# Performance work log

Measured on AMD Instinct MI355X. Metric: run time of the kernel, lower is better.

The kernel has to match this reference:

```python
import jax, jax.numpy as jnp
import numpy as np
import math

N = 100000      # num_of_nodes
E = 1600000     # edges (~avg degree 16)
F = 128         # node_feature
D = 128         # node_hidden (also topK pool size)
NR = 90000      # remaining nodes
L = 2           # num_conv_layer
LAMDA = 0.5
ALPHA = 0.1


def setup_inputs() -> dict:
    key = jax.random.key(0)
    ks = jax.random.split(key, 12)
    g = lambda k, s: jax.random.normal(k, s, jnp.float32) * 0.05
    perm = np.random.RandomState(0).permutation(N)  # disjoint remain/added split
    return {
        "x": jax.random.normal(ks[0], (N, F), jnp.float32),
        "node_scores": jax.random.normal(ks[1], (N,), jnp.float32),
        "W_hid": g(ks[2], (F, D)), "b_hid": jnp.zeros((D,), jnp.float32),
        "Wl": g(ks[3], (D, D)), "bl": jnp.zeros((D,), jnp.float32),
        "Wr": g(ks[4], (D, D)), "br": jnp.zeros((D,), jnp.float32),
        "a": g(ks[5], (1, D)),
        "h0_w": g(ks[6], (D, D)),              # initial_weight (GRU hidden init / GCN weight)
        "W_ih": g(ks[7], (3 * D, D)), "W_hh": g(ks[8], (3 * D, D)),
        "b_ih": jnp.zeros((3 * D,), jnp.float32), "b_hh": jnp.zeros((3 * D,), jnp.float32),
        "edge_index": jax.random.randint(ks[9], (2, E), 0, N),
        "remain_nodes_index": jnp.asarray(perm[:NR], jnp.int32),
        "added_nodes_index": jnp.asarray(perm[NR:], jnp.int32),
        "node_id": jnp.arange(N, dtype=jnp.int32),
    }


def _gru_step(x_in, h, W_ih, W_hh, b_ih, b_hh):
    # torch nn.GRU single step, gate order (r, z, n)
    gx = x_in @ W_ih.T + b_ih
    gh = h @ W_hh.T + b_hh
    xr, xz, xn = jnp.split(gx, 3, axis=-1)
    hr, hz, hn = jnp.split(gh, 3, axis=-1)
    r = jax.nn.sigmoid(xr + hr)
    z = jax.nn.sigmoid(xz + hz)
    n = jnp.tanh(xn + r * hn)
    return (1.0 - z) * n + z * h


def _edge_softmax_weights(edge_index, a, h_l, h_r):
    # _dynamic_self_attention_v2: per-edge scores normalized over src rows
    src, dst = edge_index[0], edge_index[1]
    al = (jax.nn.leaky_relu(h_l, 0.2) * a).sum(-1)   # [N]
    ar = (jax.nn.leaky_relu(h_r, 0.2) * a).sum(-1)   # [N]
    e = al[src] + ar[dst]                            # [E]
    e = jnp.exp(e - e.max())
    rowsum = jax.ops.segment_sum(e, src, num_segments=h_l.shape[0])
    return e / (rowsum[src] + 1e-16)


def _spmm_adj_t(edge_index, w, feats):
    # (A_trans @ feats)[i] = sum over edges with dst==i of w_e * feats[src]
    src, dst = edge_index[0], edge_index[1]
    return jax.ops.segment_sum(w[:, None] * feats[src], dst, num_segments=feats.shape[0])


def reference(x, node_scores, W_hid, b_hid, Wl, bl, Wr, br, a, h0_w, W_ih, W_hh, b_ih, b_hh, edge_index, remain_nodes_index, added_nodes_index, node_id):
    h = jax.nn.relu(x @ W_hid + b_hid)                 # [N, D]
    remain_nodes = node_id[remain_nodes_index]
    remain_x = h[remain_nodes_index]
    added_nodes = node_id[added_nodes_index]
    added_x = h[added_nodes_index]
    scores = node_scores[remain_nodes_index]
    X_res = jnp.zeros((N, D), h.dtype)
    X_res = X_res.at[remain_nodes].set(remain_x).at[added_nodes].set(added_x)
    # topK pooling branch (N > D and NR > D statically)
    _, topk = jax.lax.top_k(scores, D)
    X_pool = remain_x[topk]                            # [D, D]: GRU batch=D, feat=D
    pooling_node = remain_nodes[topk]
    h_new = _gru_step(X_pool, h0_w, W_ih, W_hh, b_ih, b_hh)  # [D, D]
    # torch: X_GCN = X_residual (alias) then in-place scatter -> both updated
    X_res = X_res.at[pooling_node].set(h_new)
    X_gcn = X_res
    Wl_X = jax.nn.relu(X_gcn @ Wl + bl)
    Wr_X = jax.nn.relu(X_gcn @ Wr + br)
    w_edge = _edge_softmax_weights(edge_index, a, Wl_X, Wr_X)
    out = X_gcn
    for l in range(1, L + 1):
        theta = math.log(LAMDA / l + 1.0)
        hi = _spmm_adj_t(edge_index, w_edge, out)
        support = (1.0 - ALPHA) * hi + ALPHA * X_res
        out = jax.nn.relu(theta * (support @ h_new) + (1.0 - theta) * support)
    return out
```

## Files before the change

### kernel.cpp

```cpp
#include <hip/hip_runtime.h>

typedef unsigned int u32;
typedef unsigned short u16;
typedef unsigned long long u64;

#define DD 128
#define ELLW 64
#define NB 196
#define BSH 9
#define BCAP 12288

typedef __attribute__((ext_vector_type(8))) short short8;
typedef __attribute__((ext_vector_type(4))) float f32x4;
union fragu { uint4 q; short8 s; };

__device__ __forceinline__ u32 mono32(float f) {
    u32 u = __float_as_uint(f);
    return (u & 0x80000000u) ? ~u : (u | 0x80000000u);
}
__device__ __forceinline__ u16 f2bf(float f) {
    u32 u = __float_as_uint(f);
    u32 r = (u + 0x7FFFu + ((u >> 16) & 1u)) >> 16;
    return (u16)r;
}
__device__ __forceinline__ float bflo(u32 p) { return __uint_as_float(p << 16); }
__device__ __forceinline__ float bfhi(u32 p) { return __uint_as_float(p & 0xFFFF0000u); }

__device__ u32 block_incl_scan(u32 v, u32* wsum ) {
    int t = threadIdx.x, lane = t & 63, wid = t >> 6;
    u32 sc = v;
#pragma unroll
    for (int off = 1; off < 64; off <<= 1) {
        u32 n1 = __shfl_up(sc, off);
        if (lane >= off) sc += n1;
    }
    if (lane == 63) wsum[wid] = sc;
    __syncthreads();
    if (t < 16) {
        u32 wv = wsum[t];
#pragma unroll
        for (int off = 1; off < 16; off <<= 1) {
            u32 n1 = __shfl_up(wv, off, 16);
            if ((t & 15) >= off) wv += n1;
        }
        wsum[t] = wv;
    }
    __syncthreads();
    u32 r = sc + (wid ? wsum[wid - 1] : 0u);
    __syncthreads();
    return r;
}

template <int MODE, int ABF>
__global__ __launch_bounds__(256) void k_mfma(
    const void* __restrict__ Ain, const float* __restrict__ B,
    const float* __restrict__ bias, const float* __restrict__ av,
    const float* __restrict__ scaleS,
    u16* __restrict__ outBF, float* __restrict__ outF, float* __restrict__ outS,
    float theta, int N) {
    __shared__ alignas(16) unsigned char As[64 * 256];
    __shared__ float spart[64];
    int t = threadIdx.x, lane = t & 63, wave = t >> 6;
    int R0 = blockIdx.x * 64;
    int brow = (lane >> 4) * 8;
    int bcol0 = wave * 32 + (lane & 15);
    fragu bfr[2][4];
#pragma unroll
    for (int ntl = 0; ntl < 2; ++ntl)
#pragma unroll
        for (int ks = 0; ks < 4; ++ks) {
            u16 h[8];
#pragma unroll
            for (int i = 0; i < 8; ++i)
                h[i] = f2bf(B[(size_t)(ks * 32 + brow + i) * 128 + bcol0 + ntl * 16]);
            bfr[ntl][ks].q = make_uint4((u32)h[0] | ((u32)h[1] << 16), (u32)h[2] | ((u32)h[3] << 16),
                                        (u32)h[4] | ((u32)h[5] << 16), (u32)h[6] | ((u32)h[7] << 16));
        }
    float bc[2] = {0.f, 0.f}, ac[2] = {0.f, 0.f};
    if (MODE == 0 || MODE == 1) {
#pragma unroll
        for (int ntl = 0; ntl < 2; ++ntl) {
            bc[ntl] = bias[bcol0 + ntl * 16];
            if (MODE == 1) ac[ntl] = av[bcol0 + ntl * 16];
        }
    }
    if (MODE == 1 && t < 64) spart[t] = 0.f;
#pragma unroll
    for (int q2 = 0; q2 < 4; ++q2) {
        int c = t + q2 * 256;
        int row = c >> 4, c16 = c & 15;
        uint4 v = make_uint4(0u, 0u, 0u, 0u);
        if (R0 + row < N) {
            if (ABF) {
                v = ((const uint4*)Ain)[(size_t)(R0 + row) * 16 + c16];
            } else {
                float4 f0 = ((const float4*)Ain)[(size_t)(R0 + row) * 32 + c16 * 2];
                float4 f1 = ((const float4*)Ain)[(size_t)(R0 + row) * 32 + c16 * 2 + 1];
                v.x = (u32)f2bf(f0.x) | ((u32)f2bf(f0.y) << 16);
                v.y = (u32)f2bf(f0.z) | ((u32)f2bf(f0.w) << 16);
                v.z = (u32)f2bf(f1.x) | ((u32)f2bf(f1.y) << 16);
                v.w = (u32)f2bf(f1.z) | ((u32)f2bf(f1.w) << 16);
            }
        }
        *(uint4*)(As + row * 256 + ((c16 * 16) ^ ((row & 7) << 4))) = v;
    }
    __syncthreads();
    int arow = lane & 15, agrp = lane >> 4;
    float om = 1.f - theta;
#pragma unroll
    for (int rs = 0; rs < 4; ++rs) {
        int rl = rs * 16 + arow;
        fragu afr[4];
#pragma unroll
        for (int ks = 0; ks < 4; ++ks)
            afr[ks].q = *(const uint4*)(As + rl * 256 + ((ks * 64 + agrp * 16) ^ ((rl & 7) << 4)));
        float part[4] = {0.f, 0.f, 0.f, 0.f};
#pragma unroll
        for (int ntl = 0; ntl < 2; ++ntl) {
            f32x4 acc = {0.f, 0.f, 0.f, 0.f};
#pragma unroll
            for (int ks = 0; ks < 4; ++ks)
                acc = __builtin_amdgcn_mfma_f32_16x16x32_bf16(afr[ks].s, bfr[ntl][ks].s, acc, 0, 0, 0);
            int colg = wave * 32 + ntl * 16 + (lane & 15);
#pragma unroll
            for (int r = 0; r < 4; ++r) {
                int rowg = R0 + rs * 16 + agrp * 4 + r;
                if (MODE == 0) {
                    float v = fmaxf(acc[r] + bc[ntl], 0.f);
                    if (rowg < N) outBF[(size_t)rowg * 128 + colg] = f2bf(v);
                } else if (MODE == 1) {
                    part[r] += fmaxf(acc[r] + bc[ntl], 0.f) * ac[ntl];
                } else {
                    int rl2 = rs * 16 + agrp * 4 + r;
                    u16 rh = *(const u16*)(As + rl2 * 256 + ((colg * 2) ^ ((rl2 & 7) << 4)));
                    float resid = __uint_as_float((u32)rh << 16);
                    float v = fmaxf(theta * acc[r] + om * resid, 0.f);
                    if (rowg < N) {
                        if (MODE == 2) {
                            float rsc = 1.f / (scaleS[rowg] + 1e-30f);
                            outBF[(size_t)rowg * 128 + colg] = f2bf(v * rsc);
                        } else {
                            outF[(size_t)rowg * 128 + colg] = v;
                        }
                    }
                }
            }
        }
        if (MODE == 1) {
#pragma unroll
            for (int r = 0; r < 4; ++r) {
                float s = part[r];
                s += __shfl_xor(s, 1); s += __shfl_xor(s, 2);
                s += __shfl_xor(s, 4); s += __shfl_xor(s, 8);
                if ((lane & 15) == 0) atomicAdd(&spart[rs * 16 + agrp * 4 + r], s);
            }
        }
    }
    if (MODE == 1) {
        __syncthreads();
        if (t < 64 && R0 + t < N) outS[R0 + t] = expf(spart[t]);
    }
}

__global__ void k_init(u32* __restrict__ curD, u32* __restrict__ curS) {
    int t = blockIdx.x * blockDim.x + threadIdx.x;
    if (t < NB) { curD[t] = (u32)t * BCAP; curS[t] = (u32)t * BCAP; }
}

__global__ __launch_bounds__(256) void k_bucket(
    const int* __restrict__ ei, u64* __restrict__ bD, u64* __restrict__ bS,
    u32* __restrict__ curD, u32* __restrict__ curS, int E, int nblocks) {
    __shared__ u32 cnt0[NB], cnt1[NB], pos0[NB], pos1[NB], base0[NB], base1[NB];
    int t = threadIdx.x;
    int chunk = (E + nblocks - 1) / nblocks;
    int e0 = blockIdx.x * chunk, e1 = min(E, e0 + chunk);
    for (int i = t; i < NB; i += 256) { cnt0[i] = 0; cnt1[i] = 0; pos0[i] = 0; pos1[i] = 0; }
    __syncthreads();
    for (int e = e0 + t; e < e1; e += 256) {
        int s = ei[e], d = ei[E + e];
        atomicAdd(&cnt0[d >> BSH], 1u);
        atomicAdd(&cnt1[s >> BSH], 1u);
    }
    __syncthreads();
    for (int i = t; i < NB; i += 256) {
        base0[i] = atomicAdd(&curD[i], cnt0[i]);
        base1[i] = atomicAdd(&curS[i], cnt1[i]);
    }
    __syncthreads();
    for (int e = e0 + t; e < e1; e += 256) {
        int s = ei[e], d = ei[E + e];
        int bd = d >> BSH, bs = s >> BSH;
        u32 pD = base0[bd] + atomicAdd(&pos0[bd], 1u);
        u32 pS = base1[bs] + atomicAdd(&pos1[bs], 1u);
        if (pD < (u32)(bd + 1) * BCAP) bD[pD] = ((u64)(u32)d << 32) | (u32)s;
        if (pS < (u32)(bs + 1) * BCAP) bS[pS] = ((u64)(u32)s << 32) | (u32)d;
    }
}

__global__ __launch_bounds__(256) void k_ell(
    const u64* __restrict__ bD, const u32* __restrict__ curD,
    int* __restrict__ ell, u32* __restrict__ cnt, int N) {
    __shared__ u32 lcnt[512];
    int b = blockIdx.x, t = threadIdx.x;
    for (int i = t; i < 512; i += 256) lcnt[i] = 0;
    __syncthreads();
    u32 beg = (u32)b * BCAP, end = curD[b];
    for (u32 e = beg + t; e < end; e += 256) {
        u64 p = bD[e];
        int d = (int)(p >> 32), s = (int)(u32)p;
        u32 q = atomicAdd(&lcnt[d & 511], 1u);
        if (q < (u32)ELLW) ell[((size_t)d << 6) + q] = s;
    }
    __syncthreads();
    int r0 = b << BSH;
    for (int i = t; i < 512; i += 256) {
        int row = r0 + i;
        if (row < N) cnt[row] = min(lcnt[i], (u32)ELLW);
    }
}

__global__ __launch_bounds__(256) void k_S(
    const u64* __restrict__ bS, const u32* __restrict__ curS,
    const float* __restrict__ ear, float* __restrict__ S, int N) {
    __shared__ float ls[512];
    int b = blockIdx.x, t = threadIdx.x;
    for (int i = t; i < 512; i += 256) ls[i] = 0.f;
    __syncthreads();
    u32 beg = (u32)b * BCAP, end = curS[b];
    for (u32 e = beg + t; e < end; e += 256) {
        u64 p = bS[e];
        int s = (int)(p >> 32), d = (int)(u32)p;
        atomicAdd(&ls[s & 511], ear[d]);
    }
    __syncthreads();
    int r0 = b << BSH;
    for (int i = t; i < 512; i += 256) {
        int row = r0 + i;
        if (row < N) S[row] = ls[i];
    }
}

__global__ void k_scale(const u32* __restrict__ Xrbf, const float* __restrict__ S,
                        u32* __restrict__ out_bf, int N) {
    int idx = blockIdx.x * blockDim.x + threadIdx.x;
    if (idx >= N * 64) return;
    int row = idx >> 6;
    float rs = 1.f / (S[row] + 1e-30f);
    u32 p = Xrbf[idx];
    out_bf[idx] = (u32)f2bf(bflo(p) * rs) | ((u32)f2bf(bfhi(p) * rs) << 16);
}

__global__ __launch_bounds__(256) void k_spmm(
    const u32* __restrict__ featsc, const u32* __restrict__ xr_bf,
    const float* __restrict__ ear, const u32* __restrict__ cnt,
    const int* __restrict__ ell, u32* __restrict__ sup_bf, int N) {
    int w = (int)((blockIdx.x * (u32)blockDim.x + threadIdx.x) >> 6);
    int lane = threadIdx.x & 63;
    if (w >= N) return;
    int m = (int)min(cnt[w], (u32)ELLW);
    int sv = (lane < m) ? ell[((size_t)w << 6) + lane] : 0;
    float a0 = 0.f, a1 = 0.f;
    int j = 0;
    for (; j + 8 <= m; j += 8) {
        int s0 = __shfl(sv, j + 0), s1 = __shfl(sv, j + 1);
        int s2 = __shfl(sv, j + 2), s3 = __shfl(sv, j + 3);
        int s4 = __shfl(sv, j + 4), s5 = __shfl(sv, j + 5);
        int s6 = __shfl(sv, j + 6), s7 = __shfl(sv, j + 7);
        u32 p0 = featsc[(size_t)s0 * 64 + lane];
        u32 p1 = featsc[(size_t)s1 * 64 + lane];
        u32 p2 = featsc[(size_t)s2 * 64 + lane];
        u32 p3 = featsc[(size_t)s3 * 64 + lane];
        u32 p4 = featsc[(size_t)s4 * 64 + lane];
        u32 p5 = featsc[(size_t)s5 * 64 + lane];
        u32 p6 = featsc[(size_t)s6 * 64 + lane];
        u32 p7 = featsc[(size_t)s7 * 64 + lane];
        a0 += bflo(p0) + bflo(p1) + bflo(p2) + bflo(p3) + bflo(p4) + bflo(p5) + bflo(p6) + bflo(p7);
        a1 += bfhi(p0) + bfhi(p1) + bfhi(p2) + bfhi(p3) + bfhi(p4) + bfhi(p5) + bfhi(p6) + bfhi(p7);
    }
    for (; j + 2 <= m; j += 2) {
        int s0 = __shfl(sv, j + 0), s1 = __shfl(sv, j + 1);
        u32 p0 = featsc[(size_t)s0 * 64 + lane];
        u32 p1 = featsc[(size_t)s1 * 64 + lane];
        a0 += bflo(p0) + bflo(p1);
        a1 += bfhi(p0) + bfhi(p1);
    }
    if (j < m) {
        int s0 = __shfl(sv, j);
        u32 p0 = featsc[(size_t)s0 * 64 + lane];
        a0 += bflo(p0);
        a1 += bfhi(p0);
    }
    float sc = 0.9f * ear[w];
    u32 xp = xr_bf[(size_t)w * 64 + lane];
    float o0 = sc * a0 + 0.1f * bflo(xp);
    float o1 = sc * a1 + 0.1f * bfhi(xp);
    sup_bf[(size_t)w * 64 + lane] = (u32)f2bf(o0) | ((u32)f2bf(o1) << 16);
}

__global__ void k_hist(const float* __restrict__ scores, const int* __restrict__ remain,
                       u32* __restrict__ hist, int NR) {
    int i = blockIdx.x * blockDim.x + threadIdx.x;
    if (i < NR) atomicAdd(&hist[mono32(scores[remain[i]]) >> 16], 1u);
}

__global__ void k_cutoff(const u32* __restrict__ hist, u32* __restrict__ misc, int K) {
    __shared__ u32 wsum[16];
    __shared__ u32 carry_s, found_s;
    int t = threadIdx.x;
    if (t == 0) { carry_s = 0; found_s = 0; }
    __syncthreads();
    for (int c = 0; c < 64; ++c) {
        int key = 65535 - ((c << 10) + t);
        u32 v = hist[key];
        u32 carry = carry_s;
        __syncthreads();
        u32 incl = block_incl_scan(v, wsum);
        u32 mycum = carry + incl;
        u32 myprev = mycum - v;
        if (mycum >= (u32)K && myprev < (u32)K) {
            misc[2] = (u32)key;
            misc[3] = myprev;
            found_s = 1;
        }
        if (t == 1023) carry_s = mycum;
        __syncthreads();
        if (found_s) return;
    }
}

__global__ void k_collect(const float* __restrict__ scores, const int* __restrict__ remain,
                          const u32* __restrict__ misc, int* __restrict__ cand,
                          u32* __restrict__ cand_cnt, int NR, int CMAX) {
    u32 B = misc[2];
    int i = blockIdx.x * blockDim.x + threadIdx.x;
    if (i < NR) {
        u32 b = mono32(scores[remain[i]]) >> 16;
        if (b >= B) {
            u32 p = atomicAdd(cand_cnt, 1u);
            if (p < (u32)CMAX) cand[p] = i;
        }
    }
}

__global__ void k_select(const float* __restrict__ scores, const int* __restrict__ remain,
                         const u32* __restrict__ misc, const int* __restrict__ cand,
                         int* __restrict__ pooling, int K, int CMAX) {
    __shared__ u64 keys[4096];
    int n = (int)min(misc[0], (u32)CMAX);
    int t = threadIdx.x;
    for (int c = t; c < n; c += 1024) {
        int i = cand[c];
        u32 m = mono32(scores[remain[i]]);
        keys[c] = ((u64)m << 32) | (u64)(0xFFFFFFFFu - (u32)i);
    }
    __syncthreads();
    for (int c = t; c < n; c += 1024) {
        u64 myk = keys[c];
        int rank = 0;
        for (int j = 0; j < n; ++j) rank += (keys[j] > myk) ? 1 : 0;
        if (rank < K) pooling[rank] = remain[cand[c]];
    }
}

__global__ void k_gru(const u16* __restrict__ Xh, const int* __restrict__ pooling,
                      const float* __restrict__ h0w, const float* __restrict__ Wih,
                      const float* __restrict__ Whh, const float* __restrict__ bih,
                      const float* __restrict__ bhh, float* __restrict__ hnew) {
    __shared__ float xrow[DD], hrow[DD];
    int j = blockIdx.x, t = threadIdx.x;
    int node = pooling[j];
    xrow[t] = __uint_as_float((u32)Xh[(size_t)node * DD + t] << 16);
    hrow[t] = h0w[j * DD + t];
    __syncthreads();
    float gx[3], gh[3];
#pragma unroll
    for (int g = 0; g < 3; ++g) {
        const float* wi = Wih + (g * DD + t) * DD;
        const float* wh = Whh + (g * DD + t) * DD;
        float ax = bih[g * DD + t];
        float ah = bhh[g * DD + t];
        for (int d = 0; d < DD; ++d) {
            ax += xrow[d] * wi[d];
            ah += hrow[d] * wh[d];
        }
        gx[g] = ax; gh[g] = ah;
    }
    float r = 1.f / (1.f + expf(-(gx[0] + gh[0])));
    float z = 1.f / (1.f + expf(-(gx[1] + gh[1])));
    float nn = tanhf(gx[2] + r * gh[2]);
    hnew[j * DD + t] = (1.f - z) * nn + z * hrow[t];
}

__global__ void k_scatter(u32* __restrict__ Xr_bf, const int* __restrict__ pooling,
                          const float* __restrict__ hnew) {
    int j = blockIdx.x, t = threadIdx.x;
    int row = pooling[j];
    float2 f = ((const float2*)hnew)[j * 64 + t];
    Xr_bf[(size_t)row * 64 + t] = (u32)f2bf(f.x) | ((u32)f2bf(f.y) << 16);
}

extern "C" void kernel_launch(void* const* d_in, const int* in_sizes, int n_in,
                              void* d_out, int out_size, void* d_ws, size_t ws_size,
                              hipStream_t stream) {
    const float* x    = (const float*)d_in[0];
    const float* nsc  = (const float*)d_in[1];
    const float* Wh   = (const float*)d_in[2];
    const float* bh   = (const float*)d_in[3];
    const float* Wr   = (const float*)d_in[6];
    const float* br   = (const float*)d_in[7];
    const float* av   = (const float*)d_in[8];
    const float* h0w  = (const float*)d_in[9];
    const float* Wih  = (const float*)d_in[10];
    const float* Whh  = (const float*)d_in[11];
    const float* bih  = (const float*)d_in[12];
    const float* bhh  = (const float*)d_in[13];
    const int* ei     = (const int*)d_in[14];
    const int* remain = (const int*)d_in[15];

    int N = in_sizes[1];
    int E = in_sizes[14] / 2;
    int NR = in_sizes[15];
    const int K = DD;
    const int CMAX = 4096;
    int mblocks = (N + 63) / 64;
    const int NBLK = 512;

    char* ws = (char*)d_ws;
    size_t off = 0;
    auto alloc = [&](size_t bytes) -> size_t {
        off = (off + 255) & ~(size_t)255;
        size_t o = off;
        off += bytes;
        return o;
    };
    size_t bucket_bytes = (size_t)2 * NB * BCAP * 8;
    size_t sup_bytes = (size_t)N * 64 * 4;
    size_t o_Xrbf = alloc((size_t)N * 64 * 4);
    size_t o_Xsc  = alloc((size_t)N * 64 * 4);
    size_t o_Abf  = alloc((size_t)N * 64 * 4);
    size_t o_sup  = alloc(bucket_bytes > sup_bytes ? bucket_bytes : sup_bytes);
    size_t o_ear  = alloc((size_t)N * 4);
    size_t o_ell  = alloc((size_t)N * ELLW * 4);
    size_t o_cand = alloc((size_t)CMAX * 4);
    size_t o_pool = alloc((size_t)K * 4);
    size_t o_hnew = alloc((size_t)DD * DD * 4);
    size_t o_S    = alloc((size_t)N * 4);
    size_t o_cnt  = alloc((size_t)N * 4);
    size_t o_cur  = alloc((size_t)2 * 256 * 4);
    size_t o_hist = alloc((size_t)65536 * 4);
    size_t o_misc = alloc((size_t)64 * 4);
    size_t zero_len = (o_misc + 64 * 4) - o_hist;
    (void)ws_size; (void)n_in; (void)out_size;

    u32*   Xrbf = (u32*)(ws + o_Xrbf);
    u32*   Xsc  = (u32*)(ws + o_Xsc);
    u32*   Abf  = (u32*)(ws + o_Abf);
    u32*   supb = (u32*)(ws + o_sup);
    u64*   bD   = (u64*)(ws + o_sup);
    u64*   bS   = (u64*)(ws + o_sup + (size_t)NB * BCAP * 8);
    float* ear  = (float*)(ws + o_ear);
    int*   ell  = (int*)(ws + o_ell);
    int*   cand = (int*)(ws + o_cand);
    int*   pool = (int*)(ws + o_pool);
    float* hnew = (float*)(ws + o_hnew);
    float* S    = (float*)(ws + o_S);
    u32*   cnt  = (u32*)(ws + o_cnt);
    u32*   curD = (u32*)(ws + o_cur);
    u32*   curS = (u32*)(ws + o_cur + 256 * 4);
    u32*   hist = (u32*)(ws + o_hist);
    u32*   misc = (u32*)(ws + o_misc);

    const float theta1 = 0.40546510810816438f;
    const float theta2 = 0.22314355131420976f;

    hipMemsetAsync(ws + o_hist, 0, zero_len, stream);

    k_mfma<0, 0><<<mblocks, 256, 0, stream>>>(x, Wh, bh, nullptr, nullptr,
                                              (u16*)Xrbf, nullptr, nullptr, 0.f, N);
    k_hist<<<(NR + 255) / 256, 256, 0, stream>>>(nsc, remain, hist, NR);
    k_cutoff<<<1, 1024, 0, stream>>>(hist, misc, K);
    k_collect<<<(NR + 255) / 256, 256, 0, stream>>>(nsc, remain, misc, cand, misc, NR, CMAX);
    k_select<<<1, 1024, 0, stream>>>(nsc, remain, misc, cand, pool, K, CMAX);
    k_gru<<<K, DD, 0, stream>>>((const u16*)Xrbf, pool, h0w, Wih, Whh, bih, bhh, hnew);
    k_scatter<<<K, 64, 0, stream>>>(Xrbf, pool, hnew);
    k_mfma<1, 1><<<mblocks, 256, 0, stream>>>(Xrbf, Wr, br, av, nullptr,
                                              nullptr, nullptr, ear, 0.f, N);
    k_init<<<1, 256, 0, stream>>>(curD, curS);
    k_bucket<<<NBLK, 256, 0, stream>>>(ei, bD, bS, curD, curS, E, NBLK);
    k_ell<<<NB, 256, 0, stream>>>(bD, curD, ell, cnt, N);
    k_S<<<NB, 256, 0, stream>>>(bS, curS, ear, S, N);
    k_scale<<<(N * 64 + 255) / 256, 256, 0, stream>>>(Xrbf, S, Xsc, N);
    k_spmm<<<(N + 3) / 4, 256, 0, stream>>>(Xsc, Xrbf, ear, cnt, ell, supb, N);
    k_mfma<2, 1><<<mblocks, 256, 0, stream>>>(supb, hnew, nullptr, nullptr, S,
                                              (u16*)Abf, nullptr, nullptr, theta1, N);
    k_spmm<<<(N + 3) / 4, 256, 0, stream>>>(Abf, Xrbf, ear, cnt, ell, supb, N);
    k_mfma<3, 1><<<mblocks, 256, 0, stream>>>(supb, hnew, nullptr, nullptr, nullptr,
                                              nullptr, (float*)d_out, nullptr, theta2, N);
}
```

Before: 382.5 us.

## Fuse SpMM gather into MFMA layer kernel and fold row scaling into S kernel

Result: slower. 522.7 us (+36.6%).

```diff
diff --git a/kernel.cpp b/kernel.cpp
--- a/kernel.cpp
+++ b/kernel.cpp
@@ -55,9 +55,7 @@
 __global__ __launch_bounds__(256) void k_mfma(
     const void* __restrict__ Ain, const float* __restrict__ B,
     const float* __restrict__ bias, const float* __restrict__ av,
-    const float* __restrict__ scaleS,
-    u16* __restrict__ outBF, float* __restrict__ outF, float* __restrict__ outS,
-    float theta, int N) {
+    u16* __restrict__ outBF, float* __restrict__ outS, int N) {
     __shared__ alignas(16) unsigned char As[64 * 256];
     __shared__ float spart[64];
     int t = threadIdx.x, lane = t & 63, wave = t >> 6;
@@ -76,13 +74,11 @@
             bfr[ntl][ks].q = make_uint4((u32)h[0] | ((u32)h[1] << 16), (u32)h[2] | ((u32)h[3] << 16),
                                         (u32)h[4] | ((u32)h[5] << 16), (u32)h[6] | ((u32)h[7] << 16));
         }
-    float bc[2] = {0.f, 0.f}, ac[2] = {0.f, 0.f};
-    if (MODE == 0 || MODE == 1) {
-#pragma unroll
-        for (int ntl = 0; ntl < 2; ++ntl) {
-            bc[ntl] = bias[bcol0 + ntl * 16];
-            if (MODE == 1) ac[ntl] = av[bcol0 + ntl * 16];
-        }
+    float bc[2], ac[2] = {0.f, 0.f};
+#pragma unroll
+    for (int ntl = 0; ntl < 2; ++ntl) {
+        bc[ntl] = bias[bcol0 + ntl * 16];
+        if (MODE == 1) ac[ntl] = av[bcol0 + ntl * 16];
     }
     if (MODE == 1 && t < 64) spart[t] = 0.f;
 #pragma unroll
@@ -106,7 +102,6 @@
     }
     __syncthreads();
     int arow = lane & 15, agrp = lane >> 4;
-    float om = 1.f - theta;
 #pragma unroll
     for (int rs = 0; rs < 4; ++rs) {
         int rl = rs * 16 + arow;
@@ -128,21 +123,8 @@
                 if (MODE == 0) {
                     float v = fmaxf(acc[r] + bc[ntl], 0.f);
                     if (rowg < N) outBF[(size_t)rowg * 128 + colg] = f2bf(v);
-                } else if (MODE == 1) {
+                } else {
                     part[r] += fmaxf(acc[r] + bc[ntl], 0.f) * ac[ntl];
-                } else {
-                    int rl2 = rs * 16 + agrp * 4 + r;
-                    u16 rh = *(const u16*)(As + rl2 * 256 + ((colg * 2) ^ ((rl2 & 7) << 4)));
-                    float resid = __uint_as_float((u32)rh << 16);
-                    float v = fmaxf(theta * acc[r] + om * resid, 0.f);
-                    if (rowg < N) {
-                        if (MODE == 2) {
-                            float rsc = 1.f / (scaleS[rowg] + 1e-30f);
-                            outBF[(size_t)rowg * 128 + colg] = f2bf(v * rsc);
-                        } else {
-                            outF[(size_t)rowg * 128 + colg] = v;
-                        }
-                    }
                 }
             }
         }
@@ -159,6 +141,97 @@
     if (MODE == 1) {
         __syncthreads();
         if (t < 64 && R0 + t < N) outS[R0 + t] = expf(spart[t]);
+    }
+}
+
+template <int MODE>
+__global__ __launch_bounds__(256) void k_layer(
+    const u32* __restrict__ feat, const u32* __restrict__ xrbf,
+    const float* __restrict__ ear, const u32* __restrict__ cnt,
+    const int* __restrict__ ell, const float* __restrict__ B,
+    const float* __restrict__ scaleS,
+    u16* __restrict__ outBF, float* __restrict__ outF, float theta, int N) {
+    __shared__ alignas(16) unsigned char As[64 * 256];
+    int t = threadIdx.x, lane = t & 63, wave = t >> 6;
+    int R0 = blockIdx.x * 64;
+    for (int r = 0; r < 16; ++r) {
+        int rowl = wave * 16 + r;
+        int rowg = R0 + rowl;
+        float a0 = 0.f, a1 = 0.f;
+        u32 pk = 0u;
+        if (rowg < N) {
+            int m = (int)min(cnt[rowg], (u32)ELLW);
+            const int* rowp = ell + ((size_t)rowg << 6);
+            int j = 0;
+            for (; j + 8 <= m; j += 8) {
+                u32 pv[8];
+#pragma unroll
+                for (int q = 0; q < 8; ++q) {
+                    int s = rowp[j + q];
+                    pv[q] = feat[(size_t)s * 64 + lane];
+                }
+#pragma unroll
+                for (int q = 0; q < 8; ++q) { a0 += bflo(pv[q]); a1 += bfhi(pv[q]); }
+            }
+            for (; j < m; ++j) {
+                int s = rowp[j];
+                u32 p = feat[(size_t)s * 64 + lane];
+                a0 += bflo(p); a1 += bfhi(p);
+            }
+            float sc = 0.9f * ear[rowg];
+            u32 xp = xrbf[(size_t)rowg * 64 + lane];
+            float o0 = sc * a0 + 0.1f * bflo(xp);
+            float o1 = sc * a1 + 0.1f * bfhi(xp);
+            pk = (u32)f2bf(o0) | ((u32)f2bf(o1) << 16);
+        }
+        *(u32*)(As + rowl * 256 + ((lane * 4) ^ ((rowl & 7) << 4))) = pk;
+    }
+    int brow = (lane >> 4) * 8, bcol0 = wave * 32 + (lane & 15);
+    fragu bfr[2][4];
+#pragma unroll
+    for (int ntl = 0; ntl < 2; ++ntl)
+#pragma unroll
+        for (int ks = 0; ks < 4; ++ks) {
+            u16 h[8];
+#pragma unroll
+            for (int i = 0; i < 8; ++i)
+                h[i] = f2bf(B[(size_t)(ks * 32 + brow + i) * 128 + bcol0 + ntl * 16]);
+            bfr[ntl][ks].q = make_uint4((u32)h[0] | ((u32)h[1] << 16), (u32)h[2] | ((u32)h[3] << 16),
+                                        (u32)h[4] | ((u32)h[5] << 16), (u32)h[6] | ((u32)h[7] << 16));
+        }
+    __syncthreads();
+    int arow = lane & 15, agrp = lane >> 4;
+    float om = 1.f - theta;
+#pragma unroll
+    for (int rs = 0; rs < 4; ++rs) {
+        int rl = rs * 16 + arow;
+        fragu afr[4];
+#pragma unroll
+        for (int ks = 0; ks < 4; ++ks)
+            afr[ks].q = *(const uint4*)(As + rl * 256 + ((ks * 64 + agrp * 16) ^ ((rl & 7) << 4)));
+#pragma unroll
+        for (int ntl = 0; ntl < 2; ++ntl) {
+            f32x4 acc = {0.f, 0.f, 0.f, 0.f};
+#pragma unroll
+            for (int ks = 0; ks < 4; ++ks)
+                acc = __builtin_amdgcn_mfma_f32_16x16x32_bf16(afr[ks].s, bfr[ntl][ks].s, acc, 0, 0, 0);
+            int colg = wave * 32 + ntl * 16 + (lane & 15);
+#pragma unroll
+            for (int r = 0; r < 4; ++r) {
+                int rowg = R0 + rs * 16 + agrp * 4 + r;
+                if (rowg >= N) continue;
+                int rl2 = rs * 16 + agrp * 4 + r;
+                u16 rh = *(const u16*)(As + rl2 * 256 + ((colg * 2) ^ ((rl2 & 7) << 4)));
+                float resid = __uint_as_float((u32)rh << 16);
+                float v = fmaxf(theta * acc[r] + om * resid, 0.f);
+                if (MODE == 2) {
+                    float rsc = 1.f / (scaleS[rowg] + 1e-30f);
+                    outBF[(size_t)rowg * 128 + colg] = f2bf(v * rsc);
+                } else {
+                    outF[(size_t)rowg * 128 + colg] = v;
+                }
+            }
+        }
     }
 }
 
@@ -219,9 +292,10 @@
     }
 }
 
-__global__ __launch_bounds__(256) void k_S(
+__global__ __launch_bounds__(256) void k_Ssc(
     const u64* __restrict__ bS, const u32* __restrict__ curS,
-    const float* __restrict__ ear, float* __restrict__ S, int N) {
+    const float* __restrict__ ear, const u32* __restrict__ Xrbf,
+    float* __restrict__ S, u32* __restrict__ Xsc, int N) {
     __shared__ float ls[512];
     int b = blockIdx.x, t = threadIdx.x;
     for (int i = t; i < 512; i += 256) ls[i] = 0.f;
@@ -238,63 +312,15 @@
         int row = r0 + i;
         if (row < N) S[row] = ls[i];
     }
-}
-
-__global__ void k_scale(const u32* __restrict__ Xrbf, const float* __restrict__ S,
-                        u32* __restrict__ out_bf, int N) {
-    int idx = blockIdx.x * blockDim.x + threadIdx.x;
-    if (idx >= N * 64) return;
-    int row = idx >> 6;
-    float rs = 1.f / (S[row] + 1e-30f);
-    u32 p = Xrbf[idx];
-    out_bf[idx] = (u32)f2bf(bflo(p) * rs) | ((u32)f2bf(bfhi(p) * rs) << 16);
-}
-
-__global__ __launch_bounds__(256) void k_spmm(
-    const u32* __restrict__ featsc, const u32* __restrict__ xr_bf,
-    const float* __restrict__ ear, const u32* __restrict__ cnt,
-    const int* __restrict__ ell, u32* __restrict__ sup_bf, int N) {
-    int w = (int)((blockIdx.x * (u32)blockDim.x + threadIdx.x) >> 6);
-    int lane = threadIdx.x & 63;
-    if (w >= N) return;
-    int m = (int)min(cnt[w], (u32)ELLW);
-    int sv = (lane < m) ? ell[((size_t)w << 6) + lane] : 0;
-    float a0 = 0.f, a1 = 0.f;
-    int j = 0;
-    for (; j + 8 <= m; j += 8) {
-        int s0 = __shfl(sv, j + 0), s1 = __shfl(sv, j + 1);
-        int s2 = __shfl(sv, j + 2), s3 = __shfl(sv, j + 3);
-        int s4 = __shfl(sv, j + 4), s5 = __shfl(sv, j + 5);
-        int s6 = __shfl(sv, j + 6), s7 = __shfl(sv, j + 7);
-        u32 p0 = featsc[(size_t)s0 * 64 + lane];
-        u32 p1 = featsc[(size_t)s1 * 64 + lane];
-        u32 p2 = featsc[(size_t)s2 * 64 + lane];
-        u32 p3 = featsc[(size_t)s3 * 64 + lane];
-        u32 p4 = featsc[(size_t)s4 * 64 + lane];
-        u32 p5 = featsc[(size_t)s5 * 64 + lane];
-        u32 p6 = featsc[(size_t)s6 * 64 + lane];
-        u32 p7 = featsc[(size_t)s7 * 64 + lane];
-        a0 += bflo(p0) + bflo(p1) + bflo(p2) + bflo(p3) + bflo(p4) + bflo(p5) + bflo(p6) + bflo(p7);
-        a1 += bfhi(p0) + bfhi(p1) + bfhi(p2) + bfhi(p3) + bfhi(p4) + bfhi(p5) + bfhi(p6) + bfhi(p7);
-    }
-    for (; j + 2 <= m; j += 2) {
-        int s0 = __shfl(sv, j + 0), s1 = __shfl(sv, j + 1);
-        u32 p0 = featsc[(size_t)s0 * 64 + lane];
-        u32 p1 = featsc[(size_t)s1 * 64 + lane];
-        a0 += bflo(p0) + bflo(p1);
-        a1 += bfhi(p0) + bfhi(p1);
-    }
-    if (j < m) {
-        int s0 = __shfl(sv, j);
-        u32 p0 = featsc[(size_t)s0 * 64 + lane];
-        a0 += bflo(p0);
-        a1 += bfhi(p0);
-    }
-    float sc = 0.9f * ear[w];
-    u32 xp = xr_bf[(size_t)w * 64 + lane];
-    float o0 = sc * a0 + 0.1f * bflo(xp);
-    float o1 = sc * a1 + 0.1f * bfhi(xp);
-    sup_bf[(size_t)w * 64 + lane] = (u32)f2bf(o0) | ((u32)f2bf(o1) << 16);
+    int rows = min(512, N - r0);
+    if (rows <= 0) return;
+    for (int idx = t; idx < rows * 64; idx += 256) {
+        int row = r0 + (idx >> 6);
+        float rs = 1.f / (ls[idx >> 6] + 1e-30f);
+        u32 p = Xrbf[(size_t)row * 64 + (idx & 63)];
+        Xsc[(size_t)row * 64 + (idx & 63)] =
+            (u32)f2bf(bflo(p) * rs) | ((u32)f2bf(bfhi(p) * rs) << 16);
+    }
 }
 
 __global__ void k_hist(const float* __restrict__ scores, const int* __restrict__ remain,
@@ -433,12 +459,10 @@
         off += bytes;
         return o;
     };
-    size_t bucket_bytes = (size_t)2 * NB * BCAP * 8;
-    size_t sup_bytes = (size_t)N * 64 * 4;
     size_t o_Xrbf = alloc((size_t)N * 64 * 4);
     size_t o_Xsc  = alloc((size_t)N * 64 * 4);
     size_t o_Abf  = alloc((size_t)N * 64 * 4);
-    size_t o_sup  = alloc(bucket_bytes > sup_bytes ? bucket_bytes : sup_bytes);
+    size_t o_bkt  = alloc((size_t)2 * NB * BCAP * 8);
     size_t o_ear  = alloc((size_t)N * 4);
     size_t o_ell  = alloc((size_t)N * ELLW * 4);
     size_t o_cand = alloc((size_t)CMAX * 4);
@@ -455,9 +479,8 @@
     u32*   Xrbf = (u32*)(ws + o_Xrbf);
     u32*   Xsc  = (u32*)(ws + o_Xsc);
     u32*   Abf  = (u32*)(ws + o_Abf);
-    u32*   supb = (u32*)(ws + o_sup);
-    u64*   bD   = (u64*)(ws + o_sup);
-    u64*   bS   = (u64*)(ws + o_sup + (size_t)NB * BCAP * 8);
+    u64*   bD   = (u64*)(ws + o_bkt);
+    u64*   bS   = (u64*)(ws + o_bkt + (size_t)NB * BCAP * 8);
     float* ear  = (float*)(ws + o_ear);
     int*   ell  = (int*)(ws + o_ell);
     int*   cand = (int*)(ws + o_cand);
@@ -475,25 +498,20 @@
 
     hipMemsetAsync(ws + o_hist, 0, zero_len, stream);
 
-    k_mfma<0, 0><<<mblocks, 256, 0, stream>>>(x, Wh, bh, nullptr, nullptr,
-                                              (u16*)Xrbf, nullptr, nullptr, 0.f, N);
+    k_mfma<0, 0><<<mblocks, 256, 0, stream>>>(x, Wh, bh, nullptr, (u16*)Xrbf, nullptr, N);
     k_hist<<<(NR + 255) / 256, 256, 0, stream>>>(nsc, remain, hist, NR);
     k_cutoff<<<1, 1024, 0, stream>>>(hist, misc, K);
     k_collect<<<(NR + 255) / 256, 256, 0, stream>>>(nsc, remain, misc, cand, misc, NR, CMAX);
     k_select<<<1, 1024, 0, stream>>>(nsc, remain, misc, cand, pool, K, CMAX);
     k_gru<<<K, DD, 0, stream>>>((const u16*)Xrbf, pool, h0w, Wih, Whh, bih, bhh, hnew);
     k_scatter<<<K, 64, 0, stream>>>(Xrbf, pool, hnew);
-    k_mfma<1, 1><<<mblocks, 256, 0, stream>>>(Xrbf, Wr, br, av, nullptr,
-                                              nullptr, nullptr, ear, 0.f, N);
+    k_mfma<1, 1><<<mblocks, 256, 0, stream>>>(Xrbf, Wr, br, av, nullptr, ear, N);
     k_init<<<1, 256, 0, stream>>>(curD, curS);
     k_bucket<<<NBLK, 256, 0, stream>>>(ei, bD, bS, curD, curS, E, NBLK);
     k_ell<<<NB, 256, 0, stream>>>(bD, curD, ell, cnt, N);
-    k_S<<<NB, 256, 0, stream>>>(bS, curS, ear, S, N);
-    k_scale<<<(N * 64 + 255) / 256, 256, 0, stream>>>(Xrbf, S, Xsc, N);
-    k_spmm<<<(N + 3) / 4, 256, 0, stream>>>(Xsc, Xrbf, ear, cnt, ell, supb, N);
-    k_mfma<2, 1><<<mblocks, 256, 0, stream>>>(supb, hnew, nullptr, nullptr, S,
-                                              (u16*)Abf, nullptr, nullptr, theta1, N);
-    k_spmm<<<(N + 3) / 4, 256, 0, stream>>>(Abf, Xrbf, ear, cnt, ell, supb, N);
-    k_mfma<3, 1><<<mblocks, 256, 0, stream>>>(supb, hnew, nullptr, nullptr, nullptr,
-                                              nullptr, (float*)d_out, nullptr, theta2, N);
-}
+    k_Ssc<<<NB, 256, 0, stream>>>(bS, curS, ear, Xrbf, S, Xsc, N);
+    k_layer<2><<<mblocks, 256, 0, stream>>>(Xsc, Xrbf, ear, cnt, ell, hnew, S,
+                                            (u16*)Abf, nullptr, theta1, N);
+    k_layer<3><<<mblocks, 256, 0, stream>>>(Abf, Xrbf, ear, cnt, ell, hnew, nullptr,
+                                            nullptr, (float*)d_out, theta2, N);
+}
```

## Slice SpMM features into column-sliced layout and fuse scaling and residual

Applied to the files above, without the earlier changes.

After: 463.4 us. 1.21x slower.

```diff
diff --git a/kernel.cpp b/kernel.cpp
--- a/kernel.cpp
+++ b/kernel.cpp
@@ -25,6 +25,9 @@
 }
 __device__ __forceinline__ float bflo(u32 p) { return __uint_as_float(p << 16); }
 __device__ __forceinline__ float bfhi(u32 p) { return __uint_as_float(p & 0xFFFF0000u); }
+__device__ __forceinline__ u32 packbf(float a, float b) {
+    return (u32)f2bf(a) | ((u32)f2bf(b) << 16);
+}
 
 __device__ u32 block_incl_scan(u32 v, u32* wsum ) {
     int t = threadIdx.x, lane = t & 63, wid = t >> 6;
@@ -53,9 +56,9 @@
 
 template <int MODE, int ABF>
 __global__ __launch_bounds__(256) void k_mfma(
-    const void* __restrict__ Ain, const float* __restrict__ B,
-    const float* __restrict__ bias, const float* __restrict__ av,
-    const float* __restrict__ scaleS,
+    const void* __restrict__ Ain, const u32* __restrict__ resid,
+    const float* __restrict__ B, const float* __restrict__ bias,
+    const float* __restrict__ av, const float* __restrict__ scaleS,
     u16* __restrict__ outBF, float* __restrict__ outF, float* __restrict__ outS,
     float theta, int N) {
     __shared__ alignas(16) unsigned char As[64 * 256];
@@ -91,15 +94,22 @@
         int row = c >> 4, c16 = c & 15;
         uint4 v = make_uint4(0u, 0u, 0u, 0u);
         if (R0 + row < N) {
-            if (ABF) {
+            if (ABF == 1) {
                 v = ((const uint4*)Ain)[(size_t)(R0 + row) * 16 + c16];
+            } else if (ABF == 2) {
+                uint4 pv = ((const uint4*)Ain)[(size_t)(R0 + row) * 16 + c16];
+                uint4 xv = ((const uint4*)resid)[(size_t)(R0 + row) * 16 + c16];
+                v.x = packbf(bflo(pv.x) + 0.1f * bflo(xv.x), bfhi(pv.x) + 0.1f * bfhi(xv.x));
+                v.y = packbf(bflo(pv.y) + 0.1f * bflo(xv.y), bfhi(pv.y) + 0.1f * bfhi(xv.y));
+                v.z = packbf(bflo(pv.z) + 0.1f * bflo(xv.z), bfhi(pv.z) + 0.1f * bfhi(xv.z));
+                v.w = packbf(bflo(pv.w) + 0.1f * bflo(xv.w), bfhi(pv.w) + 0.1f * bfhi(xv.w));
             } else {
                 float4 f0 = ((const float4*)Ain)[(size_t)(R0 + row) * 32 + c16 * 2];
                 float4 f1 = ((const float4*)Ain)[(size_t)(R0 + row) * 32 + c16 * 2 + 1];
-                v.x = (u32)f2bf(f0.x) | ((u32)f2bf(f0.y) << 16);
-                v.y = (u32)f2bf(f0.z) | ((u32)f2bf(f0.w) << 16);
-                v.z = (u32)f2bf(f1.x) | ((u32)f2bf(f1.y) << 16);
-                v.w = (u32)f2bf(f1.z) | ((u32)f2bf(f1.w) << 16);
+                v.x = packbf(f0.x, f0.y);
+                v.y = packbf(f0.z, f0.w);
+                v.z = packbf(f1.x, f1.y);
+                v.w = packbf(f1.z, f1.w);
             }
         }
         *(uint4*)(As + row * 256 + ((c16 * 16) ^ ((row & 7) << 4))) = v;
@@ -133,12 +143,12 @@
                 } else {
                     int rl2 = rs * 16 + agrp * 4 + r;
                     u16 rh = *(const u16*)(As + rl2 * 256 + ((colg * 2) ^ ((rl2 & 7) << 4)));
-                    float resid = __uint_as_float((u32)rh << 16);
-                    float v = fmaxf(theta * acc[r] + om * resid, 0.f);
+                    float resv = __uint_as_float((u32)rh << 16);
+                    float v = fmaxf(theta * acc[r] + om * resv, 0.f);
                     if (rowg < N) {
                         if (MODE == 2) {
                             float rsc = 1.f / (scaleS[rowg] + 1e-30f);
-                            outBF[(size_t)rowg * 128 + colg] = f2bf(v * rsc);
+                            outBF[((size_t)(colg >> 4) * N + rowg) * 16 + (colg & 15)] = f2bf(v * rsc);
                         } else {
                             outF[(size_t)rowg * 128 + colg] = v;
                         }
@@ -160,6 +170,45 @@
         __syncthreads();
         if (t < 64 && R0 + t < N) outS[R0 + t] = expf(spart[t]);
     }
+}
+
+__global__ __launch_bounds__(256) void k_spmm(
+    const u32* __restrict__ featS, const float* __restrict__ ear,
+    const u32* __restrict__ cnt, const int* __restrict__ ell,
+    u32* __restrict__ P, int N) {
+    int slice = blockIdx.x & 7;
+    int chunk = blockIdx.x >> 3;
+    int lane = threadIdx.x & 63, wave = threadIdx.x >> 6;
+    int r8 = lane >> 3, c8 = lane & 7;
+    int row = chunk * 32 + wave * 8 + r8;
+    if (row >= N) return;
+    int m = (int)min(cnt[row], (u32)ELLW);
+    const int* rowp = ell + ((size_t)row << 6);
+    const u32* fbase = featS + (size_t)slice * N * 8 + c8;
+    float a0 = 0.f, a1 = 0.f;
+    int j = 0;
+    for (; j + 8 <= m; j += 8) {
+        int idx = rowp[j + c8];
+        u32 pv[8];
+#pragma unroll
+        for (int q = 0; q < 8; ++q) {
+            int s = __shfl(idx, q, 8);
+            pv[q] = fbase[(size_t)s * 8];
+        }
+#pragma unroll
+        for (int q = 0; q < 8; ++q) { a0 += bflo(pv[q]); a1 += bfhi(pv[q]); }
+    }
+    int rem = m - j;
+    if (rem > 0) {
+        int idx = (c8 < rem) ? rowp[j + c8] : 0;
+        for (int q = 0; q < rem; ++q) {
+            int s = __shfl(idx, q, 8);
+            u32 p = fbase[(size_t)s * 8];
+            a0 += bflo(p); a1 += bfhi(p);
+        }
+    }
+    float sc = 0.9f * ear[row];
+    P[(size_t)row * 64 + slice * 8 + c8] = packbf(sc * a0, sc * a1);
 }
 
 __global__ void k_init(u32* __restrict__ curD, u32* __restrict__ curS) {
@@ -219,9 +268,10 @@
     }
 }
 
-__global__ __launch_bounds__(256) void k_S(
+__global__ __launch_bounds__(256) void k_Ssc(
     const u64* __restrict__ bS, const u32* __restrict__ curS,
-    const float* __restrict__ ear, float* __restrict__ S, int N) {
+    const float* __restrict__ ear, const u32* __restrict__ Xrbf,
+    float* __restrict__ S, u32* __restrict__ XscS, int N) {
     __shared__ float ls[512];
     int b = blockIdx.x, t = threadIdx.x;
     for (int i = t; i < 512; i += 256) ls[i] = 0.f;
@@ -238,63 +288,16 @@
         int row = r0 + i;
         if (row < N) S[row] = ls[i];
     }
-}
-
-__global__ void k_scale(const u32* __restrict__ Xrbf, const float* __restrict__ S,
-                        u32* __restrict__ out_bf, int N) {
-    int idx = blockIdx.x * blockDim.x + threadIdx.x;
-    if (idx >= N * 64) return;
-    int row = idx >> 6;
-    float rs = 1.f / (S[row] + 1e-30f);
-    u32 p = Xrbf[idx];
-    out_bf[idx] = (u32)f2bf(bflo(p) * rs) | ((u32)f2bf(bfhi(p) * rs) << 16);
-}
-
-__global__ __launch_bounds__(256) void k_spmm(
-    const u32* __restrict__ featsc, const u32* __restrict__ xr_bf,
-    const float* __restrict__ ear, const u32* __restrict__ cnt,
-    const int* __restrict__ ell, u32* __restrict__ sup_bf, int N) {
-    int w = (int)((blockIdx.x * (u32)blockDim.x + threadIdx.x) >> 6);
-    int lane = threadIdx.x & 63;
-    if (w >= N) return;
-    int m = (int)min(cnt[w], (u32)ELLW);
-    int sv = (lane < m) ? ell[((size_t)w << 6) + lane] : 0;
-    float a0 = 0.f, a1 = 0.f;
-    int j = 0;
-    for (; j + 8 <= m; j += 8) {
-        int s0 = __shfl(sv, j + 0), s1 = __shfl(sv, j + 1);
-        int s2 = __shfl(sv, j + 2), s3 = __shfl(sv, j + 3);
-        int s4 = __shfl(sv, j + 4), s5 = __shfl(sv, j + 5);
-        int s6 = __shfl(sv, j + 6), s7 = __shfl(sv, j + 7);
-        u32 p0 = featsc[(size_t)s0 * 64 + lane];
-        u32 p1 = featsc[(size_t)s1 * 64 + lane];
-        u32 p2 = featsc[(size_t)s2 * 64 + lane];
-        u32 p3 = featsc[(size_t)s3 * 64 + lane];
-        u32 p4 = featsc[(size_t)s4 * 64 + lane];
-        u32 p5 = featsc[(size_t)s5 * 64 + lane];
-        u32 p6 = featsc[(size_t)s6 * 64 + lane];
-        u32 p7 = featsc[(size_t)s7 * 64 + lane];
-        a0 += bflo(p0) + bflo(p1) + bflo(p2) + bflo(p3) + bflo(p4) + bflo(p5) + bflo(p6) + bflo(p7);
-        a1 += bfhi(p0) + bfhi(p1) + bfhi(p2) + bfhi(p3) + bfhi(p4) + bfhi(p5) + bfhi(p6) + bfhi(p7);
-    }
-    for (; j + 2 <= m; j += 2) {
-        int s0 = __shfl(sv, j + 0), s1 = __shfl(sv, j + 1);
-        u32 p0 = featsc[(size_t)s0 * 64 + lane];
-        u32 p1 = featsc[(size_t)s1 * 64 + lane];
-        a0 += bflo(p0) + bflo(p1);
-        a1 += bfhi(p0) + bfhi(p1);
-    }
-    if (j < m) {
-        int s0 = __shfl(sv, j);
-        u32 p0 = featsc[(size_t)s0 * 64 + lane];
-        a0 += bflo(p0);
-        a1 += bfhi(p0);
-    }
-    float sc = 0.9f * ear[w];
-    u32 xp = xr_bf[(size_t)w * 64 + lane];
-    float o0 = sc * a0 + 0.1f * bflo(xp);
-    float o1 = sc * a1 + 0.1f * bfhi(xp);
-    sup_bf[(size_t)w * 64 + lane] = (u32)f2bf(o0) | ((u32)f2bf(o1) << 16);
+    int rows = min(512, N - r0);
+    if (rows <= 0) return;
+    for (int idx = t; idx < rows * 64; idx += 256) {
+        int rl = idx >> 6, c = idx & 63;
+        int row = r0 + rl;
+        float rs = 1.f / (ls[rl] + 1e-30f);
+        u32 p = Xrbf[(size_t)row * 64 + c];
+        XscS[((size_t)(c >> 3) * N + row) * 8 + (c & 7)] =
+            packbf(bflo(p) * rs, bfhi(p) * rs);
+    }
 }
 
 __global__ void k_hist(const float* __restrict__ scores, const int* __restrict__ remain,
@@ -396,7 +399,7 @@
     int j = blockIdx.x, t = threadIdx.x;
     int row = pooling[j];
     float2 f = ((const float2*)hnew)[j * 64 + t];
-    Xr_bf[(size_t)row * 64 + t] = (u32)f2bf(f.x) | ((u32)f2bf(f.y) << 16);
+    Xr_bf[(size_t)row * 64 + t] = packbf(f.x, f.y);
 }
 
 extern "C" void kernel_launch(void* const* d_in, const int* in_sizes, int n_in,
@@ -423,6 +426,7 @@
     const int K = DD;
     const int CMAX = 4096;
     int mblocks = (N + 63) / 64;
+    int sblocks = 8 * ((N + 31) / 32);
     const int NBLK = 512;
 
     char* ws = (char*)d_ws;
@@ -455,7 +459,7 @@
     u32*   Xrbf = (u32*)(ws + o_Xrbf);
     u32*   Xsc  = (u32*)(ws + o_Xsc);
     u32*   Abf  = (u32*)(ws + o_Abf);
-    u32*   supb = (u32*)(ws + o_sup);
+    u32*   P    = (u32*)(ws + o_sup);
     u64*   bD   = (u64*)(ws + o_sup);
     u64*   bS   = (u64*)(ws + o_sup + (size_t)NB * BCAP * 8);
     float* ear  = (float*)(ws + o_ear);
@@ -475,7 +479,7 @@
 
     hipMemsetAsync(ws + o_hist, 0, zero_len, stream);
 
-    k_mfma<0, 0><<<mblocks, 256, 0, stream>>>(x, Wh, bh, nullptr, nullptr,
+    k_mfma<0, 0><<<mblocks, 256, 0, stream>>>(x, nullptr, Wh, bh, nullptr, nullptr,
                                               (u16*)Xrbf, nullptr, nullptr, 0.f, N);
     k_hist<<<(NR + 255) / 256, 256, 0, stream>>>(nsc, remain, hist, NR);
     k_cutoff<<<1, 1024, 0, stream>>>(hist, misc, K);
@@ -483,17 +487,16 @@
     k_select<<<1, 1024, 0, stream>>>(nsc, remain, misc, cand, pool, K, CMAX);
     k_gru<<<K, DD, 0, stream>>>((const u16*)Xrbf, pool, h0w, Wih, Whh, bih, bhh, hnew);
     k_scatter<<<K, 64, 0, stream>>>(Xrbf, pool, hnew);
-    k_mfma<1, 1><<<mblocks, 256, 0, stream>>>(Xrbf, Wr, br, av, nullptr,
+    k_mfma<1, 1><<<mblocks, 256, 0, stream>>>(Xrbf, nullptr, Wr, br, av, nullptr,
                                               nullptr, nullptr, ear, 0.f, N);
     k_init<<<1, 256, 0, stream>>>(curD, curS);
     k_bucket<<<NBLK, 256, 0, stream>>>(ei, bD, bS, curD, curS, E, NBLK);
     k_ell<<<NB, 256, 0, stream>>>(bD, curD, ell, cnt, N);
-    k_S<<<NB, 256, 0, stream>>>(bS, curS, ear, S, N);
-    k_scale<<<(N * 64 + 255) / 256, 256, 0, stream>>>(Xrbf, S, Xsc, N);
-    k_spmm<<<(N + 3) / 4, 256, 0, stream>>>(Xsc, Xrbf, ear, cnt, ell, supb, N);
-    k_mfma<2, 1><<<mblocks, 256, 0, stream>>>(supb, hnew, nullptr, nullptr, S,
+    k_Ssc<<<NB, 256, 0, stream>>>(bS, curS, ear, Xrbf, S, Xsc, N);
+    k_spmm<<<sblocks, 256, 0, stream>>>(Xsc, ear, cnt, ell, P, N);
+    k_mfma<2, 2><<<mblocks, 256, 0, stream>>>(P, Xrbf, hnew, nullptr, nullptr, S,
                                               (u16*)Abf, nullptr, nullptr, theta1, N);
-    k_spmm<<<(N + 3) / 4, 256, 0, stream>>>(Abf, Xrbf, ear, cnt, ell, supb, N);
-    k_mfma<3, 1><<<mblocks, 256, 0, stream>>>(supb, hnew, nullptr, nullptr, nullptr,
+    k_spmm<<<sblocks, 256, 0, stream>>>(Abf, ear, cnt, ell, P, N);
+    k_mfma<3, 2><<<mblocks, 256, 0, stream>>>(P, Xrbf, hnew, nullptr, nullptr, nullptr,
                                               nullptr, (float*)d_out, nullptr, theta2, N);
 }
```
